# Kernel tuning notes

Hardware: AMD Instinct MI355X
Metric: run time of the kernel (lower is better)

## Reference

```python
import jax, jax.numpy as jnp
import numpy as np

HIDDEN = 128
INPUT_SIZE = 64
NUM_ACTIONS = 16
BATCH = 65536


def _uniform(key, shape, scale):
    return jax.random.uniform(key, shape, jnp.float32, -scale, scale)


def setup_inputs() -> dict:
    key = jax.random.key(0)
    ks = jax.random.split(key, 14)
    s = 1.0 / np.sqrt(HIDDEN)  # pytorch LSTM/Linear init scale
    return {
        "x": jax.random.normal(ks[0], (BATCH, INPUT_SIZE), jnp.float32),
        # layer 0 LSTM weights (gate order: i, f, g, o)
        "Wih0": _uniform(ks[1], (4 * HIDDEN, INPUT_SIZE), s),
        "Whh0": _uniform(ks[2], (4 * HIDDEN, HIDDEN), s),
        "bih0": _uniform(ks[3], (4 * HIDDEN,), s),
        "bhh0": _uniform(ks[4], (4 * HIDDEN,), s),
        # layer 1 LSTM weights
        "Wih1": _uniform(ks[5], (4 * HIDDEN, HIDDEN), s),
        "Whh1": _uniform(ks[6], (4 * HIDDEN, HIDDEN), s),
        "bih1": _uniform(ks[7], (4 * HIDDEN,), s),
        "bhh1": _uniform(ks[8], (4 * HIDDEN,), s),
        # policy / value heads
        "Wp": _uniform(ks[9], (NUM_ACTIONS, HIDDEN), s),
        "bp": _uniform(ks[10], (NUM_ACTIONS,), s),
        "Wv": _uniform(ks[11], (1, HIDDEN), s),
        "bv": _uniform(ks[12], (1,), s),
    }


def _lstm_cell(x, h, c, Wih, Whh, bih, bhh):
    # gates: [B, 4H], pytorch gate order i, f, g, o
    g = x @ Wih.T + bih + h @ Whh.T + bhh
    i, f, gg, o = jnp.split(g, 4, axis=-1)
    i = jax.nn.sigmoid(i)
    f = jax.nn.sigmoid(f)
    gg = jnp.tanh(gg)
    o = jax.nn.sigmoid(o)
    c2 = f * c + i * gg
    h2 = o * jnp.tanh(c2)
    return h2, c2


def reference(x, Wih0, Whh0, bih0, bhh0, Wih1, Whh1, bih1, bhh1, Wp, bp, Wv, bv):
    B = x.shape[0]
    z = jnp.zeros((B, HIDDEN), x.dtype)  # state=None -> zero init
    # seq_len == 1: single step through the 2-layer stack
    h0, c0 = _lstm_cell(x, z, z, Wih0, Whh0, bih0, bhh0)
    h1, c1 = _lstm_cell(h0, z, z, Wih1, Whh1, bih1, bhh1)
    out = h1[None]  # [1, B, H] like pytorch LSTM output
    policy = out @ Wp.T + bp  # gumbel=True -> raw logits
    value = out @ Wv.T + bv
    return policy, value
```

## Files before the change

kernel.cpp:

```cpp
#include <hip/hip_runtime.h>
#include <hip/hip_bf16.h>

#define BATCH 65536
#define IN    64
#define H     128
#define NA    16
#define RPB   32
#define NBLK  512
#define NITER (BATCH / (NBLK * RPB))
#define HPAD  136
#define W0PAD 72

typedef __bf16 bf16x8 __attribute__((ext_vector_type(8)));
typedef float  f32x4  __attribute__((ext_vector_type(4)));

union Frag { uint4 u; bf16x8 v; };
struct F32x8 { float4 a, b; };

#define EXP2F(v) __builtin_amdgcn_exp2f(v)
#define RCPF(v)  __builtin_amdgcn_rcpf(v)
#define K1 1.442695041f
#define K2 2.885390082f

__device__ __forceinline__ F32x8 ld8f(const float* p) {
    F32x8 r;
    r.a = *reinterpret_cast<const float4*>(p);
    r.b = *reinterpret_cast<const float4*>(p + 4);
    return r;
}
__device__ __forceinline__ Frag cvt8(F32x8 x) {
    Frag f;
    f.v[0]=(__bf16)x.a.x; f.v[1]=(__bf16)x.a.y; f.v[2]=(__bf16)x.a.z; f.v[3]=(__bf16)x.a.w;
    f.v[4]=(__bf16)x.b.x; f.v[5]=(__bf16)x.b.y; f.v[6]=(__bf16)x.b.z; f.v[7]=(__bf16)x.b.w;
    return f;
}
__device__ __forceinline__ Frag g8f(const float* p) { return cvt8(ld8f(p)); }

__device__ __forceinline__ float clamp30(float v) {
    return __builtin_fminf(__builtin_fmaxf(v, -30.0f), 30.0f);
}
__device__ __forceinline__ float lstm_h(float ip, float gp, float op) {
    ip = clamp30(ip); gp = clamp30(gp); op = clamp30(op);
    const float Ei = EXP2F(-K1 * ip);
    const float Eg = EXP2F( K2 * gp);
    const float c2 = (Eg - 1.0f) * RCPF((1.0f + Ei) * (Eg + 1.0f));
    const float Eo = EXP2F(-K1 * op);
    const float Ec = EXP2F( K2 * c2);
    return (Ec - 1.0f) * RCPF((1.0f + Eo) * (Ec + 1.0f));
}

__global__ __launch_bounds__(256, 2)
void lstm_fused(const float* __restrict__ x,
                const float* __restrict__ Wih0,
                const float* __restrict__ bih0,
                const float* __restrict__ bhh0,
                const float* __restrict__ Wih1,
                const float* __restrict__ bih1,
                const float* __restrict__ bhh1,
                const float* __restrict__ Wp,
                const float* __restrict__ bp,
                const float* __restrict__ Wv,
                const float* __restrict__ bv,
                float* __restrict__ out)
{
    __shared__ __align__(16) __hip_bfloat16 w0s[4 * 6 * 16 * W0PAD];
    __shared__ __align__(16) __hip_bfloat16 hb0[RPB * HPAD];
    __shared__ __align__(16) __hip_bfloat16 hb1[RPB * HPAD];

    const int wave = threadIdx.x >> 6;
    const int lane = threadIdx.x & 63;
    const int m16  = lane & 15;
    const int quad = lane >> 4;
    const f32x4 vzero = {0.f, 0.f, 0.f, 0.f};
    const int kGoff[3] = {0, 2 * H, 3 * H};

    __hip_bfloat16* myw0 = w0s + wave * (6 * 16 * W0PAD);

#pragma unroll
    for (int ch = 0; ch < 6; ++ch) {
        const int G = ch >> 1, ci = ch & 1;
        const int grow = kGoff[G] + (wave * 2 + ci) * 16 + m16;
        const float* src = Wih0 + (size_t)grow * IN + quad * 16;
        Frag flo = g8f(src), fhi = g8f(src + 8);
        __hip_bfloat16* dst = myw0 + (ch * 16 + m16) * W0PAD + quad * 16;
        *reinterpret_cast<uint4*>(dst)     = flo.u;
        *reinterpret_cast<uint4*>(dst + 8) = fhi.u;
    }

    Frag b1[3][2][4];
#pragma unroll
    for (int G = 0; G < 3; ++G)
#pragma unroll
        for (int ci = 0; ci < 2; ++ci)
#pragma unroll
            for (int kt = 0; kt < 4; ++kt)
                b1[G][ci][kt] = g8f(Wih1 + (size_t)(kGoff[G] + (wave * 2 + ci) * 16 + m16) * H
                                    + kt * 32 + quad * 8);

    const int shead = wave & 1;
    Frag bh[4];
    float hbias;
    if (wave < 2) {
#pragma unroll
        for (int kt = 0; kt < 4; ++kt)
            bh[kt] = g8f(Wp + (size_t)m16 * H + kt * 32 + quad * 8);
        hbias = bp[m16];
    } else {
#pragma unroll
        for (int kt = 0; kt < 4; ++kt) {
            if (m16 == 0) bh[kt] = g8f(Wv + kt * 32 + quad * 8);
            else          bh[kt].u = make_uint4(0u, 0u, 0u, 0u);
        }
        hbias = bv[0];
    }

    float bi0[3][2], bi1[3][2];
#pragma unroll
    for (int G = 0; G < 3; ++G)
#pragma unroll
        for (int ci = 0; ci < 2; ++ci) {
            const int n = kGoff[G] + (wave * 2 + ci) * 16 + m16;
            bi0[G][ci] = bih0[n] + bhh0[n];
            bi1[G][ci] = bih1[n] + bhh1[n];
        }

    __syncthreads();

    F32x8 xraw[2][2];
    {
        const int r0 = blockIdx.x * RPB;
#pragma unroll
        for (int s = 0; s < 2; ++s)
#pragma unroll
            for (int kt = 0; kt < 2; ++kt)
                xraw[s][kt] = ld8f(x + (size_t)(r0 + s * 16 + m16) * IN + kt * 32 + quad * 8);
    }

    for (int it = 0; it < NITER; ++it) {
        const int rowblk = (blockIdx.x + it * NBLK) * RPB;

        Frag a1[2][2];
#pragma unroll
        for (int s = 0; s < 2; ++s)
#pragma unroll
            for (int kt = 0; kt < 2; ++kt)
                a1[s][kt] = cvt8(xraw[s][kt]);

        if (it + 1 < NITER) {
            const int r0 = (blockIdx.x + (it + 1) * NBLK) * RPB;
#pragma unroll
            for (int s = 0; s < 2; ++s)
#pragma unroll
                for (int kt = 0; kt < 2; ++kt)
                    xraw[s][kt] = ld8f(x + (size_t)(r0 + s * 16 + m16) * IN + kt * 32 + quad * 8);
        }

#pragma unroll
        for (int ci = 0; ci < 2; ++ci) {
            f32x4 acc[3][2];
#pragma unroll
            for (int G = 0; G < 3; ++G)
#pragma unroll
                for (int s = 0; s < 2; ++s) acc[G][s] = vzero;

#pragma unroll
            for (int kt = 0; kt < 2; ++kt) {
                Frag b[3];
#pragma unroll
                for (int G = 0; G < 3; ++G)
                    b[G].u = *reinterpret_cast<const uint4*>(
                        myw0 + ((G * 2 + ci) * 16 + m16) * W0PAD + kt * 32 + quad * 8);
#pragma unroll
                for (int G = 0; G < 3; ++G)
#pragma unroll
                    for (int s = 0; s < 2; ++s)
                        acc[G][s] = __builtin_amdgcn_mfma_f32_16x16x32_bf16(
                            a1[s][kt].v, b[G].v, acc[G][s], 0, 0, 0);
            }
#pragma unroll
            for (int s = 0; s < 2; ++s)
#pragma unroll
                for (int r = 0; r < 4; ++r) {
                    const float h = lstm_h(acc[0][s][r] + bi0[0][ci],
                                           acc[1][s][r] + bi0[1][ci],
                                           acc[2][s][r] + bi0[2][ci]);
                    hb0[(s * 16 + quad * 4 + r) * HPAD + (wave * 2 + ci) * 16 + m16] =
                        __float2bfloat16(h);
                }
        }
        __syncthreads();

#pragma unroll
        for (int ci = 0; ci < 2; ++ci) {
            f32x4 acc[3][2];
#pragma unroll
            for (int G = 0; G < 3; ++G)
#pragma unroll
                for (int s = 0; s < 2; ++s) acc[G][s] = vzero;

#pragma unroll
            for (int kt = 0; kt < 4; ++kt) {
                Frag a[2];
#pragma unroll
                for (int s = 0; s < 2; ++s)
                    a[s].u = *reinterpret_cast<const uint4*>(
                        hb0 + (s * 16 + m16) * HPAD + kt * 32 + quad * 8);
#pragma unroll
                for (int G = 0; G < 3; ++G)
#pragma unroll
                    for (int s = 0; s < 2; ++s)
                        acc[G][s] = __builtin_amdgcn_mfma_f32_16x16x32_bf16(
                            a[s].v, b1[G][ci][kt].v, acc[G][s], 0, 0, 0);
            }
#pragma unroll
            for (int s = 0; s < 2; ++s)
#pragma unroll
                for (int r = 0; r < 4; ++r) {
                    const float h = lstm_h(acc[0][s][r] + bi1[0][ci],
                                           acc[1][s][r] + bi1[1][ci],
                                           acc[2][s][r] + bi1[2][ci]);
                    hb1[(s * 16 + quad * 4 + r) * HPAD + (wave * 2 + ci) * 16 + m16] =
                        __float2bfloat16(h);
                }
        }
        __syncthreads();

        Frag a3[4];
#pragma unroll
        for (int kt = 0; kt < 4; ++kt)
            a3[kt].u = *reinterpret_cast<const uint4*>(
                hb1 + (shead * 16 + m16) * HPAD + kt * 32 + quad * 8);

        f32x4 ha = vzero;
#pragma unroll
        for (int kt = 0; kt < 4; ++kt)
            ha = __builtin_amdgcn_mfma_f32_16x16x32_bf16(a3[kt].v, bh[kt].v, ha, 0, 0, 0);

        if (wave < 2) {
#pragma unroll
            for (int r = 0; r < 4; ++r) {
                const int row = rowblk + shead * 16 + quad * 4 + r;
                out[(size_t)row * NA + m16] = ha[r] + hbias;
            }
        } else if (m16 == 0) {
#pragma unroll
            for (int r = 0; r < 4; ++r) {
                const int row = rowblk + shead * 16 + quad * 4 + r;
                out[(size_t)BATCH * NA + row] = ha[r] + hbias;
            }
        }
    }
}

extern "C" void kernel_launch(void* const* d_in, const int* in_sizes, int n_in,
                              void* d_out, int out_size, void* d_ws, size_t ws_size,
                              hipStream_t stream) {
    lstm_fused<<<dim3(NBLK), dim3(256), 0, stream>>>(
        (const float*)d_in[0], (const float*)d_in[1],
        (const float*)d_in[3], (const float*)d_in[4],
        (const float*)d_in[5], (const float*)d_in[7],
        (const float*)d_in[8], (const float*)d_in[9],
        (const float*)d_in[10], (const float*)d_in[11],
        (const float*)d_in[12], (float*)d_out);
}
```

Before: 119.9 us.

## Rewrite LSTM kernel as transposed per-wave MFMA chain with hidden states in registers

Each wave now owns 16 batch rows and computes the transposed gate GEMMs (weights as the A operand, activations as B), so layer outputs stay in registers as packed bf16 and feed the next layer's MFMA directly. This removes the shared-memory round trips and barriers between layers. All layer-1 and head weights are staged once per block into XOR-swizzled LDS, and the grid uses 256 blocks of 1024 threads with no per-block loop. In exchange, every block pays the full weight-staging cost, the LDS footprint is large, and register pressure is high under launch_bounds(1024,4).

Result: faster. 107.3 us (-10.5%).

```diff
diff --git a/kernel.cpp b/kernel.cpp
--- a/kernel.cpp
+++ b/kernel.cpp
@@ -5,11 +5,8 @@
 #define IN    64
 #define H     128
 #define NA    16
-#define RPB   32
-#define NBLK  512
-#define NITER (BATCH / (NBLK * RPB))
-#define HPAD  136
-#define W0PAD 72
+#define NBLK  256
+#define TPB   1024
 
 typedef __bf16 bf16x8 __attribute__((ext_vector_type(8)));
 typedef float  f32x4  __attribute__((ext_vector_type(4)));
@@ -34,8 +31,17 @@
     f.v[4]=(__bf16)x.b.x; f.v[5]=(__bf16)x.b.y; f.v[6]=(__bf16)x.b.z; f.v[7]=(__bf16)x.b.w;
     return f;
 }
-__device__ __forceinline__ Frag g8f(const float* p) { return cvt8(ld8f(p)); }
-
+__device__ __forceinline__ Frag cvt44(float4 a, float4 b) {
+    Frag f;
+    f.v[0]=(__bf16)a.x; f.v[1]=(__bf16)a.y; f.v[2]=(__bf16)a.z; f.v[3]=(__bf16)a.w;
+    f.v[4]=(__bf16)b.x; f.v[5]=(__bf16)b.y; f.v[6]=(__bf16)b.z; f.v[7]=(__bf16)b.w;
+    return f;
+}
+__device__ __forceinline__ unsigned pk2(float lo, float hi) {
+    unsigned short l = __builtin_bit_cast(unsigned short, (__bf16)lo);
+    unsigned short h = __builtin_bit_cast(unsigned short, (__bf16)hi);
+    return (unsigned)l | ((unsigned)h << 16);
+}
 __device__ __forceinline__ float clamp30(float v) {
     return __builtin_fminf(__builtin_fmaxf(v, -30.0f), 30.0f);
 }
@@ -49,7 +55,7 @@
     return (Ec - 1.0f) * RCPF((1.0f + Eo) * (Ec + 1.0f));
 }
 
-__global__ __launch_bounds__(256, 2)
+__global__ __launch_bounds__(TPB, 4)
 void lstm_fused(const float* __restrict__ x,
                 const float* __restrict__ Wih0,
                 const float* __restrict__ bih0,
@@ -63,199 +69,148 @@
                 const float* __restrict__ bv,
                 float* __restrict__ out)
 {
-    __shared__ __align__(16) __hip_bfloat16 w0s[4 * 6 * 16 * W0PAD];
-    __shared__ __align__(16) __hip_bfloat16 hb0[RPB * HPAD];
-    __shared__ __align__(16) __hip_bfloat16 hb1[RPB * HPAD];
-
-    const int wave = threadIdx.x >> 6;
-    const int lane = threadIdx.x & 63;
-    const int m16  = lane & 15;
-    const int quad = lane >> 4;
+    __shared__ __align__(16) uint4 w0s[384 * 8];
+    __shared__ __align__(16) uint4 w1s[384 * 16];
+    __shared__ __align__(16) uint4 wph[32 * 16];
+    __shared__ float b0s[384];
+    __shared__ float b1s[384];
+
+    const int tid  = threadIdx.x;
+    const int wave = tid >> 6;
+    const int lane = tid & 63;
+    const int q    = lane >> 4;
+    const int m    = lane & 15;
+    const int row  = blockIdx.x * 256 + wave * 16 + m;
     const f32x4 vzero = {0.f, 0.f, 0.f, 0.f};
-    const int kGoff[3] = {0, 2 * H, 3 * H};
-
-    __hip_bfloat16* myw0 = w0s + wave * (6 * 16 * W0PAD);
-
-#pragma unroll
-    for (int ch = 0; ch < 6; ++ch) {
-        const int G = ch >> 1, ci = ch & 1;
-        const int grow = kGoff[G] + (wave * 2 + ci) * 16 + m16;
-        const float* src = Wih0 + (size_t)grow * IN + quad * 16;
-        Frag flo = g8f(src), fhi = g8f(src + 8);
-        __hip_bfloat16* dst = myw0 + (ch * 16 + m16) * W0PAD + quad * 16;
-        *reinterpret_cast<uint4*>(dst)     = flo.u;
-        *reinterpret_cast<uint4*>(dst + 8) = fhi.u;
-    }
-
-    Frag b1[3][2][4];
-#pragma unroll
-    for (int G = 0; G < 3; ++G)
-#pragma unroll
-        for (int ci = 0; ci < 2; ++ci)
-#pragma unroll
-            for (int kt = 0; kt < 4; ++kt)
-                b1[G][ci][kt] = g8f(Wih1 + (size_t)(kGoff[G] + (wave * 2 + ci) * 16 + m16) * H
-                                    + kt * 32 + quad * 8);
-
-    const int shead = wave & 1;
-    Frag bh[4];
-    float hbias;
-    if (wave < 2) {
-#pragma unroll
-        for (int kt = 0; kt < 4; ++kt)
-            bh[kt] = g8f(Wp + (size_t)m16 * H + kt * 32 + quad * 8);
-        hbias = bp[m16];
-    } else {
+
+    const float* xp = x + (size_t)row * IN + q * 8;
+    F32x8 xr0 = ld8f(xp);
+    F32x8 xr1 = ld8f(xp + 32);
+    const float4 bpr = *reinterpret_cast<const float4*>(bp + q * 4);
+    const float  bvv = bv[0];
+
+#pragma unroll
+    for (int r = 0; r < 3; ++r) {
+        const int idx = tid + (r << 10);
+        const int j = idx >> 3, s = idx & 7;
+        const int g = j >> 7, h = j & 127;
+        const int srow = h + ((g == 0) ? 0 : (g + 1) * 128);
+        Frag f = cvt8(ld8f(Wih0 + (size_t)srow * IN + s * 8));
+        w0s[(j << 3) + (s ^ (j & 7))] = f.u;
+    }
+#pragma unroll
+    for (int r = 0; r < 6; ++r) {
+        const int idx = tid + (r << 10);
+        const int j = idx >> 4, s = idx & 15;
+        const int g = j >> 7, h = j & 127;
+        const int srow = h + ((g == 0) ? 0 : (g + 1) * 128);
+        const int kt = s >> 2, qq = s & 3;
+        const float* pA = Wih1 + (size_t)srow * H + kt * 32 + qq * 4;
+        Frag f = cvt44(*reinterpret_cast<const float4*>(pA),
+                       *reinterpret_cast<const float4*>(pA + 16));
+        w1s[(j << 4) + (s ^ (j & 7))] = f.u;
+    }
+    if (tid < 512) {
+        const int j = tid >> 4, s = tid & 15;
+        const int kt = s >> 2, qq = s & 3;
+        Frag f;
+        if (j <= 16) {
+            const float* base = (j < 16) ? (Wp + (size_t)j * H) : Wv;
+            const float* pA = base + kt * 32 + qq * 4;
+            f = cvt44(*reinterpret_cast<const float4*>(pA),
+                      *reinterpret_cast<const float4*>(pA + 16));
+        } else {
+            f.u = make_uint4(0u, 0u, 0u, 0u);
+        }
+        wph[(j << 4) + (s ^ (j & 7))] = f.u;
+    }
+    if (tid < 384) {
+        const int g = tid >> 7, h = tid & 127;
+        const int srow = h + ((g == 0) ? 0 : (g + 1) * 128);
+        b0s[tid] = bih0[srow] + bhh0[srow];
+    } else if (tid < 768) {
+        const int t = tid - 384;
+        const int g = t >> 7, h = t & 127;
+        const int srow = h + ((g == 0) ? 0 : (g + 1) * 128);
+        b1s[t] = bih1[srow] + bhh1[srow];
+    }
+
+    __syncthreads();
+
+    const int swz = m & 7;
+    Frag xb[2];
+    xb[0] = cvt8(xr0);
+    xb[1] = cvt8(xr1);
+
+    unsigned hw0[16];
+#pragma unroll
+    for (int nc = 0; nc < 8; ++nc) {
+        f32x4 acc[3]; acc[0] = vzero; acc[1] = vzero; acc[2] = vzero;
+#pragma unroll
+        for (int g = 0; g < 3; ++g) {
+            const int n = g * 128 + nc * 16 + m;
+#pragma unroll
+            for (int kt = 0; kt < 2; ++kt) {
+                Frag a; a.u = w0s[(n << 3) + ((kt * 4 + q) ^ swz)];
+                acc[g] = __builtin_amdgcn_mfma_f32_16x16x32_bf16(a.v, xb[kt].v, acc[g], 0, 0, 0);
+            }
+        }
+        const f32x4 bI = *reinterpret_cast<const f32x4*>(b0s +       nc * 16 + q * 4);
+        const f32x4 bG = *reinterpret_cast<const f32x4*>(b0s + 128 + nc * 16 + q * 4);
+        const f32x4 bO = *reinterpret_cast<const f32x4*>(b0s + 256 + nc * 16 + q * 4);
+#pragma unroll
+        for (int u = 0; u < 2; ++u) {
+            const float ha = lstm_h(acc[0][2*u]   + bI[2*u],   acc[1][2*u]   + bG[2*u],   acc[2][2*u]   + bO[2*u]);
+            const float hb = lstm_h(acc[0][2*u+1] + bI[2*u+1], acc[1][2*u+1] + bG[2*u+1], acc[2][2*u+1] + bO[2*u+1]);
+            hw0[nc * 2 + u] = pk2(ha, hb);
+        }
+    }
+
+    unsigned hw1[16];
+#pragma unroll
+    for (int nc = 0; nc < 8; ++nc) {
+        f32x4 acc[3]; acc[0] = vzero; acc[1] = vzero; acc[2] = vzero;
 #pragma unroll
         for (int kt = 0; kt < 4; ++kt) {
-            if (m16 == 0) bh[kt] = g8f(Wv + kt * 32 + quad * 8);
-            else          bh[kt].u = make_uint4(0u, 0u, 0u, 0u);
-        }
-        hbias = bv[0];
-    }
-
-    float bi0[3][2], bi1[3][2];
-#pragma unroll
-    for (int G = 0; G < 3; ++G)
-#pragma unroll
-        for (int ci = 0; ci < 2; ++ci) {
-            const int n = kGoff[G] + (wave * 2 + ci) * 16 + m16;
-            bi0[G][ci] = bih0[n] + bhh0[n];
-            bi1[G][ci] = bih1[n] + bhh1[n];
-        }
-
-    __syncthreads();
-
-    F32x8 xraw[2][2];
-    {
-        const int r0 = blockIdx.x * RPB;
-#pragma unroll
-        for (int s = 0; s < 2; ++s)
-#pragma unroll
-            for (int kt = 0; kt < 2; ++kt)
-                xraw[s][kt] = ld8f(x + (size_t)(r0 + s * 16 + m16) * IN + kt * 32 + quad * 8);
-    }
-
-    for (int it = 0; it < NITER; ++it) {
-        const int rowblk = (blockIdx.x + it * NBLK) * RPB;
-
-        Frag a1[2][2];
-#pragma unroll
-        for (int s = 0; s < 2; ++s)
-#pragma unroll
-            for (int kt = 0; kt < 2; ++kt)
-                a1[s][kt] = cvt8(xraw[s][kt]);
-
-        if (it + 1 < NITER) {
-            const int r0 = (blockIdx.x + (it + 1) * NBLK) * RPB;
-#pragma unroll
-            for (int s = 0; s < 2; ++s)
-#pragma unroll
-                for (int kt = 0; kt < 2; ++kt)
-                    xraw[s][kt] = ld8f(x + (size_t)(r0 + s * 16 + m16) * IN + kt * 32 + quad * 8);
-        }
-
-#pragma unroll
-        for (int ci = 0; ci < 2; ++ci) {
-            f32x4 acc[3][2];
-#pragma unroll
-            for (int G = 0; G < 3; ++G)
-#pragma unroll
-                for (int s = 0; s < 2; ++s) acc[G][s] = vzero;
-
-#pragma unroll
-            for (int kt = 0; kt < 2; ++kt) {
-                Frag b[3];
-#pragma unroll
-                for (int G = 0; G < 3; ++G)
-                    b[G].u = *reinterpret_cast<const uint4*>(
-                        myw0 + ((G * 2 + ci) * 16 + m16) * W0PAD + kt * 32 + quad * 8);
-#pragma unroll
-                for (int G = 0; G < 3; ++G)
-#pragma unroll
-                    for (int s = 0; s < 2; ++s)
-                        acc[G][s] = __builtin_amdgcn_mfma_f32_16x16x32_bf16(
-                            a1[s][kt].v, b[G].v, acc[G][s], 0, 0, 0);
+            Frag b; b.u = make_uint4(hw0[4*kt], hw0[4*kt+1], hw0[4*kt+2], hw0[4*kt+3]);
+#pragma unroll
+            for (int g = 0; g < 3; ++g) {
+                const int n = g * 128 + nc * 16 + m;
+                Frag a; a.u = w1s[(n << 4) + ((kt * 4 + q) ^ swz)];
+                acc[g] = __builtin_amdgcn_mfma_f32_16x16x32_bf16(a.v, b.v, acc[g], 0, 0, 0);
             }
-#pragma unroll
-            for (int s = 0; s < 2; ++s)
-#pragma unroll
-                for (int r = 0; r < 4; ++r) {
-                    const float h = lstm_h(acc[0][s][r] + bi0[0][ci],
-                                           acc[1][s][r] + bi0[1][ci],
-                                           acc[2][s][r] + bi0[2][ci]);
-                    hb0[(s * 16 + quad * 4 + r) * HPAD + (wave * 2 + ci) * 16 + m16] =
-                        __float2bfloat16(h);
-                }
-        }
-        __syncthreads();
-
-#pragma unroll
-        for (int ci = 0; ci < 2; ++ci) {
-            f32x4 acc[3][2];
-#pragma unroll
-            for (int G = 0; G < 3; ++G)
-#pragma unroll
-                for (int s = 0; s < 2; ++s) acc[G][s] = vzero;
-
-#pragma unroll
-            for (int kt = 0; kt < 4; ++kt) {
-                Frag a[2];
-#pragma unroll
-                for (int s = 0; s < 2; ++s)
-                    a[s].u = *reinterpret_cast<const uint4*>(
-                        hb0 + (s * 16 + m16) * HPAD + kt * 32 + quad * 8);
-#pragma unroll
-                for (int G = 0; G < 3; ++G)
-#pragma unroll
-                    for (int s = 0; s < 2; ++s)
-                        acc[G][s] = __builtin_amdgcn_mfma_f32_16x16x32_bf16(
-                            a[s].v, b1[G][ci][kt].v, acc[G][s], 0, 0, 0);
-            }
-#pragma unroll
-            for (int s = 0; s < 2; ++s)
-#pragma unroll
-                for (int r = 0; r < 4; ++r) {
-                    const float h = lstm_h(acc[0][s][r] + bi1[0][ci],
-                                           acc[1][s][r] + bi1[1][ci],
-                                           acc[2][s][r] + bi1[2][ci]);
-                    hb1[(s * 16 + quad * 4 + r) * HPAD + (wave * 2 + ci) * 16 + m16] =
-                        __float2bfloat16(h);
-                }
-        }
-        __syncthreads();
-
-        Frag a3[4];
-#pragma unroll
-        for (int kt = 0; kt < 4; ++kt)
-            a3[kt].u = *reinterpret_cast<const uint4*>(
-                hb1 + (shead * 16 + m16) * HPAD + kt * 32 + quad * 8);
-
-        f32x4 ha = vzero;
-#pragma unroll
-        for (int kt = 0; kt < 4; ++kt)
-            ha = __builtin_amdgcn_mfma_f32_16x16x32_bf16(a3[kt].v, bh[kt].v, ha, 0, 0, 0);
-
-        if (wave < 2) {
-#pragma unroll
-            for (int r = 0; r < 4; ++r) {
-                const int row = rowblk + shead * 16 + quad * 4 + r;
-                out[(size_t)row * NA + m16] = ha[r] + hbias;
-            }
-        } else if (m16 == 0) {
-#pragma unroll
-            for (int r = 0; r < 4; ++r) {
-                const int row = rowblk + shead * 16 + quad * 4 + r;
-                out[(size_t)BATCH * NA + row] = ha[r] + hbias;
-            }
-        }
-    }
+        }
+        const f32x4 bI = *reinterpret_cast<const f32x4*>(b1s +       nc * 16 + q * 4);
+        const f32x4 bG = *reinterpret_cast<const f32x4*>(b1s + 128 + nc * 16 + q * 4);
+        const f32x4 bO = *reinterpret_cast<const f32x4*>(b1s + 256 + nc * 16 + q * 4);
+#pragma unroll
+        for (int u = 0; u < 2; ++u) {
+            const float ha = lstm_h(acc[0][2*u]   + bI[2*u],   acc[1][2*u]   + bG[2*u],   acc[2][2*u]   + bO[2*u]);
+            const float hb = lstm_h(acc[0][2*u+1] + bI[2*u+1], acc[1][2*u+1] + bG[2*u+1], acc[2][2*u+1] + bO[2*u+1]);
+            hw1[nc * 2 + u] = pk2(ha, hb);
+        }
+    }
+
+    f32x4 ap = vzero, av = vzero;
+#pragma unroll
+    for (int kt = 0; kt < 4; ++kt) {
+        Frag b; b.u = make_uint4(hw1[4*kt], hw1[4*kt+1], hw1[4*kt+2], hw1[4*kt+3]);
+        Frag a0; a0.u = wph[( m       << 4) + ((kt * 4 + q) ^ swz)];
+        ap = __builtin_amdgcn_mfma_f32_16x16x32_bf16(a0.v, b.v, ap, 0, 0, 0);
+        Frag a1; a1.u = wph[((16 + m) << 4) + ((kt * 4 + q) ^ swz)];
+        av = __builtin_amdgcn_mfma_f32_16x16x32_bf16(a1.v, b.v, av, 0, 0, 0);
+    }
+    f32x4 po;
+    po[0] = ap[0] + bpr.x; po[1] = ap[1] + bpr.y;
+    po[2] = ap[2] + bpr.z; po[3] = ap[3] + bpr.w;
+    *reinterpret_cast<f32x4*>(out + (size_t)row * NA + q * 4) = po;
+    if (q == 0) out[(size_t)BATCH * NA + row] = av[0] + bvv;
 }
 
 extern "C" void kernel_launch(void* const* d_in, const int* in_sizes, int n_in,
                               void* d_out, int out_size, void* d_ws, size_t ws_size,
                               hipStream_t stream) {
-    lstm_fused<<<dim3(NBLK), dim3(256), 0, stream>>>(
+    lstm_fused<<<dim3(NBLK), dim3(TPB), 0, stream>>>(
         (const float*)d_in[0], (const float*)d_in[1],
         (const float*)d_in[3], (const float*)d_in[4],
         (const float*)d_in[5], (const float*)d_in[7],
```
